# Kernel optimization log

Hardware: AMD Instinct MI355X
Metric: run time of the kernel (lower is better)

## Reference

```python
import jax, jax.numpy as jnp
import numpy as np

N_EMBED = 256
N_HEAD = 8
HEAD = N_EMBED // N_HEAD
LN_EPS = 1e-5


def _layernorm(x, g, b):
    mu = jnp.mean(x, axis=-1, keepdims=True)
    var = jnp.mean(jnp.square(x - mu), axis=-1, keepdims=True)
    return (x - mu) * jax.lax.rsqrt(var + LN_EPS) * g + b


def setup_inputs() -> dict:
    key = jax.random.key(0)
    ks = jax.random.split(key, 12)
    B, T, C, H, D = 16, 1024, N_EMBED, N_HEAD, HEAD
    s = C ** -0.5
    return {
        "x": jax.random.normal(ks[0], (B, T, C), jnp.float32),
        "wq": jax.random.normal(ks[1], (H, C, D), jnp.float32) * s,
        "wk": jax.random.normal(ks[2], (H, C, D), jnp.float32) * s,
        "wv": jax.random.normal(ks[3], (H, C, D), jnp.float32) * s,
        "w_proj": jax.random.normal(ks[4], (C, C), jnp.float32) * s,
        "b_proj": jnp.zeros((C,), jnp.float32),
        "w1": jax.random.normal(ks[5], (C, 4 * C), jnp.float32) * s,
        "b1": jnp.zeros((4 * C,), jnp.float32),
        "w2": jax.random.normal(ks[6], (4 * C, C), jnp.float32) * (4 * C) ** -0.5,
        "b2": jnp.zeros((C,), jnp.float32),
        "ln1_g": jnp.ones((C,), jnp.float32),
        "ln1_b": jnp.zeros((C,), jnp.float32),
        "ln2_g": jnp.ones((C,), jnp.float32),
        "ln2_b": jnp.zeros((C,), jnp.float32),
    }


def reference(x, wq, wk, wv, w_proj, b_proj, w1, b1, w2, b2,
              ln1_g, ln1_b, ln2_g, ln2_b):
    B, T, C = x.shape
    # --- multi-head causal self-attention on ln1(x) ---
    h = _layernorm(x, ln1_g, ln1_b)
    q = jnp.einsum('btc,hcd->bhtd', h, wq)
    k = jnp.einsum('btc,hcd->bhtd', h, wk)
    v = jnp.einsum('btc,hcd->bhtd', h, wv)
    # NOTE: original scales by n_embed**-0.5 (C of input), not head_size
    wei = jnp.einsum('bhtd,bhsd->bhts', q, k) * (C ** -0.5)
    causal = jnp.tril(jnp.ones((T, T), bool))
    wei = jnp.where(causal, wei, -jnp.inf)
    wei = jax.nn.softmax(wei, axis=-1)
    att = jnp.einsum('bhts,bhsd->bhtd', wei, v)
    att = att.transpose(0, 2, 1, 3).reshape(B, T, C)  # concat heads
    x = x + att @ w_proj + b_proj
    # --- feedforward on ln2(x) ---
    h2 = _layernorm(x, ln2_g, ln2_b)
    f = jax.nn.relu(h2 @ w1 + b1) @ w2 + b2
    return x + f
```

## Files before the change

### kernel.cpp

```cpp
#include <hip/hip_runtime.h>


typedef unsigned short u16;
typedef unsigned int u32;
typedef __attribute__((ext_vector_type(8))) short short8v;
typedef __attribute__((ext_vector_type(4))) float float4v;

__device__ __forceinline__ float b2f(u16 u) { union { u32 i; float f; } v; v.i = (u32)u << 16; return v.f; }
__device__ __forceinline__ float lo2f(u32 u) { union { u32 i; float f; } v; v.i = u << 16; return v.f; }
__device__ __forceinline__ float hi2f(u32 u) { union { u32 i; float f; } v; v.i = u & 0xffff0000u; return v.f; }
__device__ __forceinline__ u16 f2b(float f) {
    union { float f; u32 i; } v; v.f = f;
    u32 r = v.i + 0x7fffu + ((v.i >> 16) & 1u);
    return (u16)(r >> 16);
}
__device__ __forceinline__ u32 pk2_rtz(float a, float b) {
    return (__float_as_uint(a) >> 16) | (__float_as_uint(b) & 0xffff0000u);
}
__device__ __forceinline__ void async_cp16(const u16* g, u16* l) {
    __builtin_amdgcn_global_load_lds((const __attribute__((address_space(1))) void*)g,
                                     (__attribute__((address_space(3))) void*)l, 16, 0, 0);
}

__global__ __launch_bounds__(256) void prep_ln1(const float* __restrict__ wq,
                                                const float* __restrict__ wk,
                                                const float* __restrict__ wv,
                                                const float* __restrict__ wp,
                                                const float* __restrict__ w1,
                                                const float* __restrict__ w2,
                                                const float* __restrict__ x,
                                                const float* __restrict__ g1,
                                                const float* __restrict__ be1,
                                                u16* __restrict__ wqkvT,
                                                u16* __restrict__ wpT,
                                                u16* __restrict__ w1T,
                                                u16* __restrict__ w2T,
                                                u16* __restrict__ hout) {
    __shared__ u16 tile[64][65];
    int bid = blockIdx.x, tid = threadIdx.x;
    if (bid < 768) {
        int i = bid * 256 + tid;
        int n = i >> 8, k = i & 255;
        int which = n >> 8, nn = n & 255;
        const float* w = which == 0 ? wq : (which == 1 ? wk : wv);
        float v = w[((nn >> 5) * 256 + k) * 32 + (nn & 31)];
        if (which == 0) v *= 0.09016844f;
        wqkvT[i] = f2b(v);
    } else if (bid < 912) {
        const float* src; u16* dst; int K, N, t;
        if (bid < 784)      { src = wp; dst = wpT; K = 256;  N = 256;  t = bid - 768; }
        else if (bid < 848) { src = w1; dst = w1T; K = 256;  N = 1024; t = bid - 784; }
        else                { src = w2; dst = w2T; K = 1024; N = 256;  t = bid - 848; }
        int ntn = N >> 6;
        int k0 = (t / ntn) << 6, n0 = (t % ntn) << 6;
        int lane = tid & 63, wrow = tid >> 6;
        #pragma unroll
        for (int r = 0; r < 16; r++) {
            int k = wrow * 16 + r;
            tile[k][lane] = f2b(src[(size_t)(k0 + k) * N + n0 + lane]);
        }
        __syncthreads();
        #pragma unroll
        for (int r = 0; r < 16; r++) {
            int n = wrow * 16 + r;
            dst[(size_t)(n0 + n) * K + k0 + lane] = tile[lane][n];
        }
    } else {
        int row = (bid - 912) * 4 + (tid >> 6);
        int lane = tid & 63;
        float4 xv = *(const float4*)(x + (size_t)row * 256 + lane * 4);
        float v0 = xv.x, v1 = xv.y, v2 = xv.z, v3 = xv.w;
        float s = v0 + v1 + v2 + v3;
        #pragma unroll
        for (int m = 32; m; m >>= 1) s += __shfl_xor(s, m);
        float mu = s * 0.00390625f;
        float d0 = v0 - mu, d1 = v1 - mu, d2 = v2 - mu, d3 = v3 - mu;
        float ss = d0 * d0 + d1 * d1 + d2 * d2 + d3 * d3;
        #pragma unroll
        for (int m = 32; m; m >>= 1) ss += __shfl_xor(ss, m);
        float rs = rsqrtf(ss * 0.00390625f + 1e-5f);
        float4 g = *(const float4*)(g1 + lane * 4);
        float4 b = *(const float4*)(be1 + lane * 4);
        uint2 r;
        r.x = (u32)f2b(d0 * rs * g.x + b.x) | ((u32)f2b(d1 * rs * g.y + b.y) << 16);
        r.y = (u32)f2b(d2 * rs * g.z + b.z) | ((u32)f2b(d3 * rs * g.w + b.w) << 16);
        *(uint2*)(hout + (size_t)row * 256 + lane * 4) = r;
    }
}

template<bool HASBIAS, bool RELU, bool QKV>
__global__ __launch_bounds__(256) void gemm128(const u16* __restrict__ A,
                                               const u16* __restrict__ Bt,
                                               const float* __restrict__ bias,
                                               u16* __restrict__ out,
                                               u16* __restrict__ vout,
                                               int M, int N, int K) {
    __shared__ __align__(16) u16 SH[32768];
    const int tid = threadIdx.x, lane = tid & 63, w = tid >> 6;
    const int m0 = blockIdx.x * 128, n0 = blockIdx.y * 128;
    const int wm = (w & 1) * 64, wn = (w >> 1) * 64;
    const int fm = lane & 15, q = lane >> 4;

    float4v acc[4][4];
    #pragma unroll
    for (int i = 0; i < 4; i++)
        #pragma unroll
        for (int j = 0; j < 4; j++) acc[i][j] = (float4v){0.f, 0.f, 0.f, 0.f};

    const int kset = ((lane & 7) ^ (lane >> 3)) * 8;
    const u16* Ag = A  + (size_t)(m0 + w * 32 + (lane >> 3)) * K + kset;
    const u16* Bg = Bt + (size_t)(n0 + w * 32 + (lane >> 3)) * K + kset;

    auto issueS = [&](int t, int d) {
        u16* Asw = SH + d * 16384 + (w * 32) * 64;
        u16* Bsw = SH + d * 16384 + 8192 + (w * 32) * 64;
        #pragma unroll
        for (int c = 0; c < 4; c++) {
            async_cp16(Ag + (size_t)c * 8 * K + t * 64, Asw + c * 8 * 64);
            async_cp16(Bg + (size_t)c * 8 * K + t * 64, Bsw + c * 8 * 64);
        }
    };
    issueS(0, 0);
    issueS(1, 1);

    const int sw = fm & 7;
    #pragma unroll
    for (int t = 0; t < 4; ++t) {
        if (t == 3) asm volatile("s_waitcnt vmcnt(0)" ::: "memory");
        else        asm volatile("s_waitcnt vmcnt(8)" ::: "memory");
        __builtin_amdgcn_s_barrier();
        const u16* As = SH + (t & 1) * 16384;
        const u16* Bs = As + 8192;
        __builtin_amdgcn_s_setprio(1);
        #pragma unroll
        for (int kk = 0; kk < 64; kk += 32) {
            const int slot = (((kk >> 3) + q) ^ sw) * 8;
            short8v af[4], bf[4];
            #pragma unroll
            for (int mi = 0; mi < 4; mi++)
                af[mi] = *(const short8v*)&As[(wm + mi * 16 + fm) * 64 + slot];
            #pragma unroll
            for (int ni = 0; ni < 4; ni++)
                bf[ni] = *(const short8v*)&Bs[(wn + ni * 16 + fm) * 64 + slot];
            #pragma unroll
            for (int mi = 0; mi < 4; mi++)
                #pragma unroll
                for (int ni = 0; ni < 4; ni++)
                    acc[mi][ni] = __builtin_amdgcn_mfma_f32_16x16x32_bf16(
                        bf[ni], af[mi], acc[mi][ni], 0, 0, 0);
        }
        __builtin_amdgcn_s_setprio(0);
        if (t < 2) {
            __builtin_amdgcn_s_barrier();
            issueS(t + 2, t & 1);
        }
    }

    if (QKV && n0 >= 512) {
        __syncthreads();
        #pragma unroll
        for (int mi = 0; mi < 4; mi++) {
            int ml = wm + mi * 16 + fm;
            #pragma unroll
            for (int ni = 0; ni < 4; ni++) {
                int nl = wn + ni * 16 + q * 4;
                #pragma unroll
                for (int r = 0; r < 4; r++)
                    SH[(nl + r) * 136 + ml] = f2b(acc[mi][ni][r]);
            }
        }
        __syncthreads();
        int r = tid & 127, c = (tid >> 7) << 6;
        int hd = (n0 - 512) + r;
        int b = m0 >> 10, t0 = m0 & 1023;
        u16* dst = vout + (size_t)(b * 256 + hd) * 1024 + t0 + c;
        const u16* srcT = SH + r * 136 + c;
        #pragma unroll
        for (int i = 0; i < 8; i++)
            *(uint4*)(dst + i * 8) = *(const uint4*)(srcT + i * 8);
        return;
    }

    #pragma unroll
    for (int mi = 0; mi < 4; mi++) {
        int row = m0 + wm + mi * 16 + fm;
        #pragma unroll
        for (int ni = 0; ni < 4; ni++) {
            int nb = n0 + wn + ni * 16 + q * 4;
            float v0 = acc[mi][ni][0], v1 = acc[mi][ni][1],
                  v2 = acc[mi][ni][2], v3 = acc[mi][ni][3];
            if (HASBIAS) {
                float4 bv = *(const float4*)&bias[nb];
                v0 += bv.x; v1 += bv.y; v2 += bv.z; v3 += bv.w;
            }
            if (RELU) {
                v0 = fmaxf(v0, 0.f); v1 = fmaxf(v1, 0.f);
                v2 = fmaxf(v2, 0.f); v3 = fmaxf(v3, 0.f);
            }
            size_t idx = (size_t)row * N + nb;
            uint2 ov;
            ov.x = (u32)f2b(v0) | ((u32)f2b(v1) << 16);
            ov.y = (u32)f2b(v2) | ((u32)f2b(v3) << 16);
            *(uint2*)&out[idx] = ov;
        }
    }
}

__global__ __launch_bounds__(512, 1) void tail_fused(const u16* __restrict__ att,
                                                     const u16* __restrict__ wpT,
                                                     const float* __restrict__ bp,
                                                     const float* __restrict__ x,
                                                     const float* __restrict__ g2,
                                                     const float* __restrict__ be2,
                                                     const u16* __restrict__ w1T,
                                                     const float* __restrict__ b1,
                                                     const u16* __restrict__ w2T,
                                                     const float* __restrict__ b2,
                                                     float* __restrict__ out) {
    __shared__ __align__(16) u16 SH[65536];
    __shared__ float ps[2][2][16][4], pq[2][2][16][4];
    u16* Ms = SH;
    u16* Bs = SH + 16384;
    const int tid = threadIdx.x, lane = tid & 63, w = tid >> 6;
    const int m0 = blockIdx.x * 64;
    const int wmi = w & 1, wni = w >> 1;
    const int wm = wmi * 32;
    const int wn = wni * 64;
    const int fm = lane & 15, q = lane >> 4;
    const int sw = fm & 7;
    const int kset = ((lane & 7) ^ (lane >> 3)) * 8;
    const int rb = w * 8 + (lane >> 3);

    short8v ar[8][2];
    {
        const u16* Abase = att + (size_t)(m0 + wm + fm) * 256 + q * 8;
        #pragma unroll
        for (int kcn = 0; kcn < 8; kcn++)
            #pragma unroll
            for (int mi = 0; mi < 2; mi++)
                ar[kcn][mi] = *(const short8v*)(Abase + (size_t)mi * 16 * 256 + kcn * 32);
    }

    auto issueB = [&](int u, u16* dst) {
        if (u < 4) {
            const u16* src = wpT + (size_t)rb * 256 + u * 64 + kset;
            #pragma unroll
            for (int c = 0; c < 4; c++)
                async_cp16(src + (size_t)c * 64 * 256, dst + c * 4096);
        } else {
            const int tt = u - 4, n2 = tt >> 3, k2 = tt & 3;
            if (((tt >> 2) & 1) == 0) {
                const u16* src = w1T + (size_t)(n2 * 256 + rb) * 256 + k2 * 64 + kset;
                #pragma unroll
                for (int c = 0; c < 4; c++)
                    async_cp16(src + (size_t)c * 64 * 256, dst + c * 4096);
            } else {
                const u16* src = w2T + (size_t)rb * 1024 + n2 * 256 + k2 * 64 + kset;
                #pragma unroll
                for (int c = 0; c < 4; c++)
                    async_cp16(src + (size_t)c * 64 * 1024, dst + c * 4096);
            }
        }
    };

    issueB(0, Bs + w * 512);
    issueB(1, Bs + 16384 + w * 512);

    float4v acc1[2][4], acc2[2][4], xr[2][4];
    #pragma unroll
    for (int i = 0; i < 2; i++)
        #pragma unroll
        for (int j = 0; j < 4; j++) {
            acc1[i][j] = (float4v){0.f, 0.f, 0.f, 0.f};
            acc2[i][j] = (float4v){0.f, 0.f, 0.f, 0.f};
        }

    #pragma unroll
    for (int t = 0; t < 36; ++t) {
        if (t == 35) asm volatile("s_waitcnt vmcnt(0)" ::: "memory");
        else         asm volatile("s_waitcnt vmcnt(4)" ::: "memory");
        __builtin_amdgcn_s_barrier();
        if (t + 2 < 36)
            issueB(t + 2, Bs + ((t + 2) % 3) * 16384 + w * 512);
        const u16* Bb = Bs + (t % 3) * 16384;

        if (t < 4) {
            __builtin_amdgcn_s_setprio(1);
            #pragma unroll
            for (int kk = 0; kk < 64; kk += 32) {
                const int slot = (((kk >> 3) + q) ^ sw) * 8;
                short8v bf[4];
                #pragma unroll
                for (int ni = 0; ni < 4; ni++)
                    bf[ni] = *(const short8v*)&Bb[(wn + ni * 16 + fm) * 64 + slot];
                #pragma unroll
                for (int mi = 0; mi < 2; mi++)
                    #pragma unroll
                    for (int ni = 0; ni < 4; ni++)
                        acc1[mi][ni] = __builtin_amdgcn_mfma_f32_16x16x32_bf16(
                            bf[ni], ar[t * 2 + (kk >> 5)][mi], acc1[mi][ni], 0, 0, 0);
            }
            __builtin_amdgcn_s_setprio(0);
            if (t == 3) {
                float s[2] = {0.f, 0.f}, s2[2] = {0.f, 0.f};
                #pragma unroll
                for (int mi = 0; mi < 2; mi++)
                    #pragma unroll
                    for (int ni = 0; ni < 4; ni++) {
                        const int nb = wn + ni * 16 + q * 4;
                        const int row = m0 + wm + mi * 16 + fm;
                        float4 bv = *(const float4*)&bp[nb];
                        float4 xv = *(const float4*)(x + (size_t)row * 256 + nb);
                        #pragma unroll
                        for (int r = 0; r < 4; r++) {
                            float tv = acc1[mi][ni][r] + (&bv.x)[r] + (&xv.x)[r];
                            xr[mi][ni][r] = tv;
                            s[mi] += tv; s2[mi] += tv * tv;
                        }
                    }
                #pragma unroll
                for (int mi = 0; mi < 2; mi++) {
                    s[mi]  += __shfl_xor(s[mi], 16);  s[mi]  += __shfl_xor(s[mi], 32);
                    s2[mi] += __shfl_xor(s2[mi], 16); s2[mi] += __shfl_xor(s2[mi], 32);
                }
                if (q == 0) {
                    ps[wmi][0][fm][wni] = s[0];  ps[wmi][1][fm][wni] = s[1];
                    pq[wmi][0][fm][wni] = s2[0]; pq[wmi][1][fm][wni] = s2[1];
                }
                asm volatile("s_waitcnt lgkmcnt(0)" ::: "memory");
                __builtin_amdgcn_s_barrier();
                float mu[2], rs[2];
                #pragma unroll
                for (int mi = 0; mi < 2; mi++) {
                    float S  = ps[wmi][mi][fm][0] + ps[wmi][mi][fm][1]
                             + ps[wmi][mi][fm][2] + ps[wmi][mi][fm][3];
                    float SQ = pq[wmi][mi][fm][0] + pq[wmi][mi][fm][1]
                             + pq[wmi][mi][fm][2] + pq[wmi][mi][fm][3];
                    mu[mi] = S * 0.00390625f;
                    rs[mi] = rsqrtf(SQ * 0.00390625f - mu[mi] * mu[mi] + 1e-5f);
                }
                #pragma unroll
                for (int ni = 0; ni < 4; ni++) {
                    const int c2 = wn + ni * 16 + q * 4;
                    const int kcM = c2 >> 6, cc = c2 & 63;
                    float4 gv = *(const float4*)&g2[c2];
                    float4 bv = *(const float4*)&be2[c2];
                    #pragma unroll
                    for (int mi = 0; mi < 2; mi++) {
                        const int row = wm + mi * 16 + fm;
                        float h0 = (xr[mi][ni][0] - mu[mi]) * rs[mi] * gv.x + bv.x;
                        float h1 = (xr[mi][ni][1] - mu[mi]) * rs[mi] * gv.y + bv.y;
                        float h2v = (xr[mi][ni][2] - mu[mi]) * rs[mi] * gv.z + bv.z;
                        float h3 = (xr[mi][ni][3] - mu[mi]) * rs[mi] * gv.w + bv.w;
                        uint2 pp;
                        pp.x = (u32)f2b(h0) | ((u32)f2b(h1) << 16);
                        pp.y = (u32)f2b(h2v) | ((u32)f2b(h3) << 16);
                        *(uint2*)&Ms[kcM * 4096 + row * 64 +
                                     (((cc >> 3) ^ (row & 7)) * 8) + (cc & 7)] = pp;
                    }
                }
                asm volatile("s_waitcnt lgkmcnt(0)" ::: "memory");
                __builtin_amdgcn_s_barrier();
                #pragma unroll
                for (int kcn = 0; kcn < 8; kcn++) {
                    const int kcq = kcn >> 1, kk = (kcn & 1) * 32;
                    const int slot = (((kk >> 3) + q) ^ sw) * 8;
                    #pragma unroll
                    for (int mi = 0; mi < 2; mi++)
                        ar[kcn][mi] = *(const short8v*)&Ms[kcq * 4096 +
                                        (wm + mi * 16 + fm) * 64 + slot];
                }
            }
        } else {
            const int tt = t - 4;
            const int nch = tt >> 3, ph = (tt >> 2) & 1, kc = tt & 3;
            if (ph == 0) {
                if (kc == 0) {
                    #pragma unroll
                    for (int i = 0; i < 2; i++)
                        #pragma unroll
                        for (int j = 0; j < 4; j++) acc1[i][j] = (float4v){0.f, 0.f, 0.f, 0.f};
                }
                __builtin_amdgcn_s_setprio(1);
                #pragma unroll
                for (int kk = 0; kk < 64; kk += 32) {
                    const int slot = (((kk >> 3) + q) ^ sw) * 8;
                    short8v bf[4];
                    #pragma unroll
                    for (int ni = 0; ni < 4; ni++)
                        bf[ni] = *(const short8v*)&Bb[(wn + ni * 16 + fm) * 64 + slot];
                    #pragma unroll
                    for (int mi = 0; mi < 2; mi++)
                        #pragma unroll
                        for (int ni = 0; ni < 4; ni++)
                            acc1[mi][ni] = __builtin_amdgcn_mfma_f32_16x16x32_bf16(
                                bf[ni], ar[kc * 2 + (kk >> 5)][mi], acc1[mi][ni], 0, 0, 0);
                }
                __builtin_amdgcn_s_setprio(0);
                if (kc == 3) {
                    #pragma unroll
                    for (int ni = 0; ni < 4; ni++) {
                        const int c2 = wn + ni * 16 + q * 4;
                        const int kcM = c2 >> 6, cc = c2 & 63;
                        float4 bv = *(const float4*)&b1[nch * 256 + c2];
                        #pragma unroll
                        for (int mi = 0; mi < 2; mi++) {
                            const int row = wm + mi * 16 + fm;
                            float v0 = fmaxf(acc1[mi][ni][0] + bv.x, 0.f);
                            float v1 = fmaxf(acc1[mi][ni][1] + bv.y, 0.f);
                            float v2 = fmaxf(acc1[mi][ni][2] + bv.z, 0.f);
                            float v3 = fmaxf(acc1[mi][ni][3] + bv.w, 0.f);
                            uint2 pp;
                            pp.x = (u32)f2b(v0) | ((u32)f2b(v1) << 16);
                            pp.y = (u32)f2b(v2) | ((u32)f2b(v3) << 16);
                            *(uint2*)&Ms[kcM * 4096 + row * 64 +
                                         (((cc >> 3) ^ (row & 7)) * 8) + (cc & 7)] = pp;
                        }
                    }
                    asm volatile("s_waitcnt lgkmcnt(0)" ::: "memory");
                }
            } else {
                const u16* Ab = Ms + kc * 4096;
                __builtin_amdgcn_s_setprio(1);
                #pragma unroll
                for (int kk = 0; kk < 64; kk += 32) {
                    const int slot = (((kk >> 3) + q) ^ sw) * 8;
                    short8v af[2], bf[4];
                    #pragma unroll
                    for (int mi = 0; mi < 2; mi++)
                        af[mi] = *(const short8v*)&Ab[(wm + mi * 16 + fm) * 64 + slot];
                    #pragma unroll
                    for (int ni = 0; ni < 4; ni++)
                        bf[ni] = *(const short8v*)&Bb[(wn + ni * 16 + fm) * 64 + slot];
                    #pragma unroll
                    for (int mi = 0; mi < 2; mi++)
                        #pragma unroll
                        for (int ni = 0; ni < 4; ni++)
                            acc2[mi][ni] = __builtin_amdgcn_mfma_f32_16x16x32_bf16(
                                bf[ni], af[mi], acc2[mi][ni], 0, 0, 0);
                }
                __builtin_amdgcn_s_setprio(0);
            }
        }
    }

    #pragma unroll
    for (int mi = 0; mi < 2; mi++) {
        const int row = m0 + wm + mi * 16 + fm;
        #pragma unroll
        for (int ni = 0; ni < 4; ni++) {
            const int nb = wn + ni * 16 + q * 4;
            size_t idx = (size_t)row * 256 + nb;
            float4 bv = *(const float4*)&b2[nb];
            float v0 = acc2[mi][ni][0] + bv.x + xr[mi][ni][0];
            float v1 = acc2[mi][ni][1] + bv.y + xr[mi][ni][1];
            float v2 = acc2[mi][ni][2] + bv.z + xr[mi][ni][2];
            float v3 = acc2[mi][ni][3] + bv.w + xr[mi][ni][3];
            *(float4*)&out[idx] = (float4){v0, v1, v2, v3};
        }
    }
}

__global__ __launch_bounds__(256) void attn_mfma(const u16* __restrict__ qk,
                                                 const u16* __restrict__ vtg,
                                                 u16* __restrict__ att) {
    const int T = 1024;
    int jj = (blockIdx.x + (blockIdx.y >> 3)) & 7;
    int b = blockIdx.y >> 3, hh = blockIdx.y & 7;
    int tid = threadIdx.x;
    int lane = tid & 63, w = tid >> 6;
    int fm = lane & 15, q = lane >> 4;

    __shared__ __align__(16) u16 Ks[2][64][72];
    __shared__ __align__(16) u16 Vt[2][32][72];
    __shared__ __align__(16) u16 Pl[4][16][72];

    size_t base = (size_t)b * T * 512;
    const u16* kb = qk + base + 256 + hh * 32;
    const u16* vt = vtg + (size_t)((b * 8 + hh) * 32) * 1024;
    const int krow = tid >> 2, kcol = (tid & 3) * 8;
    const int vd = tid >> 3, vs = (tid & 7) * 8;

    int qa0 = jj * 64, qb0 = (15 - jj) * 64;
    int tqa = qa0 + w * 16 + fm, tqb = qb0 + w * 16 + fm;
    short8v qfa = *(const short8v*)(qk + base + (size_t)tqa * 512 + hh * 32 + q * 8);
    short8v qfb = *(const short8v*)(qk + base + (size_t)tqb * 512 + hh * 32 + q * 8);
    float4v oa0 = {0.f, 0.f, 0.f, 0.f}, oa1 = {0.f, 0.f, 0.f, 0.f};
    float4v ob0 = {0.f, 0.f, 0.f, 0.f}, ob1 = {0.f, 0.f, 0.f, 0.f};
    float la = 0.f, lb = 0.f;
    int wqa = qa0 + w * 16, wqb = qb0 + w * 16;
    int nIter = 16 - jj;

    uint4 kreg = *(const uint4*)(kb + (size_t)krow * 512 + kcol);
    uint4 vreg = *(const uint4*)(vt + (size_t)vd * 1024 + vs);

    for (int it = 0; it < nIter; ++it) {
        int s0 = it << 6;
        const int cb = it & 1;
        *(uint4*)&Ks[cb][krow][kcol] = kreg;
        *(uint4*)&Vt[cb][vd][vs] = vreg;
        if (it + 1 < nIter) {
            int ns0 = s0 + 64;
            kreg = *(const uint4*)(kb + (size_t)(ns0 + krow) * 512 + kcol);
            vreg = *(const uint4*)(vt + (size_t)vd * 1024 + ns0 + vs);
        }
        asm volatile("s_waitcnt lgkmcnt(0)" ::: "memory");
        __builtin_amdgcn_s_barrier();
        short8v kf0 = *(const short8v*)&Ks[cb][fm][q * 8];
        short8v kf1 = *(const short8v*)&Ks[cb][16 + fm][q * 8];
        short8v kf2 = *(const short8v*)&Ks[cb][32 + fm][q * 8];
        short8v kf3 = *(const short8v*)&Ks[cb][48 + fm][q * 8];
        short8v vf00 = *(const short8v*)&Vt[cb][fm][q * 8];
        short8v vf01 = *(const short8v*)&Vt[cb][fm][32 + q * 8];
        short8v vf10 = *(const short8v*)&Vt[cb][16 + fm][q * 8];
        short8v vf11 = *(const short8v*)&Vt[cb][16 + fm][32 + q * 8];
        float4v z = {0.f, 0.f, 0.f, 0.f};

        #pragma unroll
        for (int t2 = 0; t2 < 2; t2++) {
            int wq0 = t2 ? wqa : wqb;
            if (s0 >= wq0 + 16) continue;
            int tq = t2 ? tqa : tqb;
            short8v qf = t2 ? qfa : qfb;
            __builtin_amdgcn_s_setprio(1);
            float4v s_0 = __builtin_amdgcn_mfma_f32_16x16x32_bf16(kf0, qf, z, 0, 0, 0);
            float4v s_1 = __builtin_amdgcn_mfma_f32_16x16x32_bf16(kf1, qf, z, 0, 0, 0);
            float4v s_2 = __builtin_amdgcn_mfma_f32_16x16x32_bf16(kf2, qf, z, 0, 0, 0);
            float4v s_3 = __builtin_amdgcn_mfma_f32_16x16x32_bf16(kf3, qf, z, 0, 0, 0);
            __builtin_amdgcn_s_setprio(0);
            float p[16];
            #pragma unroll
            for (int r = 0; r < 4; r++) {
                p[r] = exp2f(s_0[r]); p[4 + r] = exp2f(s_1[r]);
                p[8 + r] = exp2f(s_2[r]); p[12 + r] = exp2f(s_3[r]);
            }
            if (s0 + 63 > wq0) {
                int sb = s0 + q * 4;
                #pragma unroll
                for (int c = 0; c < 4; c++)
                    #pragma unroll
                    for (int r = 0; r < 4; r++)
                        if (sb + c * 16 + r > tq) p[c * 4 + r] = 0.f;
            }
            float rsum = 0.f;
            #pragma unroll
            for (int i = 0; i < 16; i++) rsum += p[i];
            rsum += __shfl_xor(rsum, 16);
            rsum += __shfl_xor(rsum, 32);
            if (t2) la += rsum; else lb += rsum;

            #pragma unroll
            for (int c = 0; c < 4; c++) {
                uint2 pp;
                pp.x = pk2_rtz(p[c * 4 + 0], p[c * 4 + 1]);
                pp.y = pk2_rtz(p[c * 4 + 2], p[c * 4 + 3]);
                *(uint2*)&Pl[w][fm][c * 16 + q * 4] = pp;
            }
            short8v pf0 = *(const short8v*)&Pl[w][fm][q * 8];
            short8v pf1 = *(const short8v*)&Pl[w][fm][32 + q * 8];
            __builtin_amdgcn_s_setprio(1);
            if (t2) {
                oa0 = __builtin_amdgcn_mfma_f32_16x16x32_bf16(vf00, pf0, oa0, 0, 0, 0);
                oa0 = __builtin_amdgcn_mfma_f32_16x16x32_bf16(vf01, pf1, oa0, 0, 0, 0);
                oa1 = __builtin_amdgcn_mfma_f32_16x16x32_bf16(vf10, pf0, oa1, 0, 0, 0);
                oa1 = __builtin_amdgcn_mfma_f32_16x16x32_bf16(vf11, pf1, oa1, 0, 0, 0);
            } else {
                ob0 = __builtin_amdgcn_mfma_f32_16x16x32_bf16(vf00, pf0, ob0, 0, 0, 0);
                ob0 = __builtin_amdgcn_mfma_f32_16x16x32_bf16(vf01, pf1, ob0, 0, 0, 0);
                ob1 = __builtin_amdgcn_mfma_f32_16x16x32_bf16(vf10, pf0, ob1, 0, 0, 0);
                ob1 = __builtin_amdgcn_mfma_f32_16x16x32_bf16(vf11, pf1, ob1, 0, 0, 0);
            }
            __builtin_amdgcn_s_setprio(0);
        }
    }

    #pragma unroll
    for (int t2 = 0; t2 < 2; t2++) {
        float inv = 1.f / (t2 ? la : lb);
        float4v o0 = t2 ? oa0 : ob0, o1 = t2 ? oa1 : ob1;
        int tq = t2 ? tqa : tqb;
        uint2 r0, r1;
        r0.x = (u32)f2b(o0[0] * inv) | ((u32)f2b(o0[1] * inv) << 16);
        r0.y = (u32)f2b(o0[2] * inv) | ((u32)f2b(o0[3] * inv) << 16);
        r1.x = (u32)f2b(o1[0] * inv) | ((u32)f2b(o1[1] * inv) << 16);
        r1.y = (u32)f2b(o1[2] * inv) | ((u32)f2b(o1[3] * inv) << 16);
        size_t o = (size_t)(b * T + tq) * 256 + hh * 32;
        *(uint2*)(att + o + q * 4) = r0;
        *(uint2*)(att + o + 16 + q * 4) = r1;
    }
}

extern "C" void kernel_launch(void* const* d_in, const int* in_sizes, int n_in,
                              void* d_out, int out_size, void* d_ws, size_t ws_size,
                              hipStream_t stream) {
    const int BT = 16 * 1024;
    const float* x      = (const float*)d_in[0];
    const float* wq     = (const float*)d_in[1];
    const float* wk     = (const float*)d_in[2];
    const float* wv     = (const float*)d_in[3];
    const float* w_proj = (const float*)d_in[4];
    const float* b_proj = (const float*)d_in[5];
    const float* w1     = (const float*)d_in[6];
    const float* b1     = (const float*)d_in[7];
    const float* w2     = (const float*)d_in[8];
    const float* b2     = (const float*)d_in[9];
    const float* ln1_g  = (const float*)d_in[10];
    const float* ln1_b  = (const float*)d_in[11];
    const float* ln2_g  = (const float*)d_in[12];
    const float* ln2_b  = (const float*)d_in[13];

    char* ws = (char*)d_ws;
    const size_t MB = 1024 * 1024;
    u16*  hbuf  = (u16*)(ws + 8 * MB);
    u16*  qk    = (u16*)(ws + 16 * MB);
    u16*  vtg   = (u16*)(ws + 32 * MB);
    u16*  wqkvT = (u16*)(ws + 48 * MB);
    u16*  wpT   = (u16*)(ws + 48 * MB + 0x60000);
    u16*  w1T   = (u16*)(ws + 48 * MB + 0x80000);
    u16*  w2T   = (u16*)(ws + 48 * MB + 0x100000);

    prep_ln1<<<5008, 256, 0, stream>>>(wq, wk, wv, w_proj, w1, w2, x, ln1_g, ln1_b,
                                       wqkvT, wpT, w1T, w2T, hbuf);
    gemm128<false, false, true><<<dim3(128, 6), 256, 0, stream>>>(
        hbuf, wqkvT, nullptr, qk, vtg, BT, 512, 256);
    attn_mfma<<<dim3(8, 128), 256, 0, stream>>>(qk, vtg, hbuf);
    tail_fused<<<256, 512, 0, stream>>>(hbuf, wpT, b_proj, x, ln2_g, ln2_b,
                                        w1T, b1, w2T, b2, (float*)d_out);
}
```

Before: 174.3 us.

## Split weight prefetch across MMA halves and batch QK MFMAs in attention

In the fused tail kernel, each per-stage weight prefetch is split into two halves. The second half is issued between the two k-halves of the MFMA work, so global-to-LDS copies are spread through compute instead of bunched after the barrier. In the attention kernel, the QK score MFMAs for both query sub-tiles are issued together before either softmax/PV sequence, which lets the MFMA pipeline overlap with the exp work. The b-tile is now computed unconditionally, which assumes it is always active. It also raises register pressure from holding eight score fragments at once.

```diff
diff --git a/kernel.cpp b/kernel.cpp
--- a/kernel.cpp
+++ b/kernel.cpp
@@ -206,6 +206,39 @@
     }
 }
 
+#define TMM_A(KH, AFRAG, ACC)                                                     \
+    do {                                                                          \
+        const int slot_ = ((((KH) ? 4 : 0) + q) ^ sw) * 8;                        \
+        short8v bf_[4];                                                           \
+        _Pragma("unroll")                                                         \
+        for (int ni = 0; ni < 4; ni++)                                            \
+            bf_[ni] = *(const short8v*)&Bb[(wn + ni * 16 + fm) * 64 + slot_];     \
+        _Pragma("unroll")                                                         \
+        for (int mi = 0; mi < 2; mi++)                                            \
+            _Pragma("unroll")                                                     \
+            for (int ni = 0; ni < 4; ni++)                                        \
+                ACC[mi][ni] = __builtin_amdgcn_mfma_f32_16x16x32_bf16(            \
+                    bf_[ni], (AFRAG), ACC[mi][ni], 0, 0, 0);                      \
+    } while (0)
+
+#define TMM_M(KH, ABASE, ACC)                                                     \
+    do {                                                                          \
+        const int slot_ = ((((KH) ? 4 : 0) + q) ^ sw) * 8;                        \
+        short8v af_[2], bf_[4];                                                   \
+        _Pragma("unroll")                                                         \
+        for (int mi = 0; mi < 2; mi++)                                            \
+            af_[mi] = *(const short8v*)&(ABASE)[(wm + mi * 16 + fm) * 64 + slot_];\
+        _Pragma("unroll")                                                         \
+        for (int ni = 0; ni < 4; ni++)                                            \
+            bf_[ni] = *(const short8v*)&Bb[(wn + ni * 16 + fm) * 64 + slot_];     \
+        _Pragma("unroll")                                                         \
+        for (int mi = 0; mi < 2; mi++)                                            \
+            _Pragma("unroll")                                                     \
+            for (int ni = 0; ni < 4; ni++)                                        \
+                ACC[mi][ni] = __builtin_amdgcn_mfma_f32_16x16x32_bf16(            \
+                    bf_[ni], af_[mi], ACC[mi][ni], 0, 0, 0);                      \
+    } while (0)
+
 __global__ __launch_bounds__(512, 1) void tail_fused(const u16* __restrict__ att,
                                                      const u16* __restrict__ wpT,
                                                      const float* __restrict__ bp,
@@ -241,30 +274,31 @@
                 ar[kcn][mi] = *(const short8v*)(Abase + (size_t)mi * 16 * 256 + kcn * 32);
     }
 
-    auto issueB = [&](int u, u16* dst) {
+    auto issueBh = [&](int u, u16* dst, int h) {
+        const int c0 = h * 2;
         if (u < 4) {
             const u16* src = wpT + (size_t)rb * 256 + u * 64 + kset;
             #pragma unroll
-            for (int c = 0; c < 4; c++)
+            for (int c = c0; c < c0 + 2; c++)
                 async_cp16(src + (size_t)c * 64 * 256, dst + c * 4096);
         } else {
             const int tt = u - 4, n2 = tt >> 3, k2 = tt & 3;
             if (((tt >> 2) & 1) == 0) {
                 const u16* src = w1T + (size_t)(n2 * 256 + rb) * 256 + k2 * 64 + kset;
                 #pragma unroll
-                for (int c = 0; c < 4; c++)
+                for (int c = c0; c < c0 + 2; c++)
                     async_cp16(src + (size_t)c * 64 * 256, dst + c * 4096);
             } else {
                 const u16* src = w2T + (size_t)rb * 1024 + n2 * 256 + k2 * 64 + kset;
                 #pragma unroll
-                for (int c = 0; c < 4; c++)
+                for (int c = c0; c < c0 + 2; c++)
                     async_cp16(src + (size_t)c * 64 * 1024, dst + c * 4096);
             }
         }
     };
 
-    issueB(0, Bs + w * 512);
-    issueB(1, Bs + 16384 + w * 512);
+    issueBh(0, Bs + w * 512, 0); issueBh(0, Bs + w * 512, 1);
+    issueBh(1, Bs + 16384 + w * 512, 0); issueBh(1, Bs + 16384 + w * 512, 1);
 
     float4v acc1[2][4], acc2[2][4], xr[2][4];
     #pragma unroll
@@ -280,26 +314,18 @@
         if (t == 35) asm volatile("s_waitcnt vmcnt(0)" ::: "memory");
         else         asm volatile("s_waitcnt vmcnt(4)" ::: "memory");
         __builtin_amdgcn_s_barrier();
-        if (t + 2 < 36)
-            issueB(t + 2, Bs + ((t + 2) % 3) * 16384 + w * 512);
+        u16* dstB = Bs + ((t + 2) % 3) * 16384 + w * 512;
+        const bool doIss = (t + 2 < 36);
+        if (doIss) issueBh(t + 2, dstB, 0);
         const u16* Bb = Bs + (t % 3) * 16384;
 
         if (t < 4) {
             __builtin_amdgcn_s_setprio(1);
-            #pragma unroll
-            for (int kk = 0; kk < 64; kk += 32) {
-                const int slot = (((kk >> 3) + q) ^ sw) * 8;
-                short8v bf[4];
-                #pragma unroll
-                for (int ni = 0; ni < 4; ni++)
-                    bf[ni] = *(const short8v*)&Bb[(wn + ni * 16 + fm) * 64 + slot];
-                #pragma unroll
-                for (int mi = 0; mi < 2; mi++)
-                    #pragma unroll
-                    for (int ni = 0; ni < 4; ni++)
-                        acc1[mi][ni] = __builtin_amdgcn_mfma_f32_16x16x32_bf16(
-                            bf[ni], ar[t * 2 + (kk >> 5)][mi], acc1[mi][ni], 0, 0, 0);
-            }
+            TMM_A(0, ar[t * 2 + 0][mi], acc1);
+            __builtin_amdgcn_s_setprio(0);
+            if (doIss) issueBh(t + 2, dstB, 1);
+            __builtin_amdgcn_s_setprio(1);
+            TMM_A(1, ar[t * 2 + 1][mi], acc1);
             __builtin_amdgcn_s_setprio(0);
             if (t == 3) {
                 float s[2] = {0.f, 0.f}, s2[2] = {0.f, 0.f};
@@ -382,20 +408,11 @@
                         for (int j = 0; j < 4; j++) acc1[i][j] = (float4v){0.f, 0.f, 0.f, 0.f};
                 }
                 __builtin_amdgcn_s_setprio(1);
-                #pragma unroll
-                for (int kk = 0; kk < 64; kk += 32) {
-                    const int slot = (((kk >> 3) + q) ^ sw) * 8;
-                    short8v bf[4];
-                    #pragma unroll
-                    for (int ni = 0; ni < 4; ni++)
-                        bf[ni] = *(const short8v*)&Bb[(wn + ni * 16 + fm) * 64 + slot];
-                    #pragma unroll
-                    for (int mi = 0; mi < 2; mi++)
-                        #pragma unroll
-                        for (int ni = 0; ni < 4; ni++)
-                            acc1[mi][ni] = __builtin_amdgcn_mfma_f32_16x16x32_bf16(
-                                bf[ni], ar[kc * 2 + (kk >> 5)][mi], acc1[mi][ni], 0, 0, 0);
-                }
+                TMM_A(0, ar[kc * 2 + 0][mi], acc1);
+                __builtin_amdgcn_s_setprio(0);
+                if (doIss) issueBh(t + 2, dstB, 1);
+                __builtin_amdgcn_s_setprio(1);
+                TMM_A(1, ar[kc * 2 + 1][mi], acc1);
                 __builtin_amdgcn_s_setprio(0);
                 if (kc == 3) {
                     #pragma unroll
@@ -422,23 +439,11 @@
             } else {
                 const u16* Ab = Ms + kc * 4096;
                 __builtin_amdgcn_s_setprio(1);
-                #pragma unroll
-                for (int kk = 0; kk < 64; kk += 32) {
-                    const int slot = (((kk >> 3) + q) ^ sw) * 8;
-                    short8v af[2], bf[4];
-                    #pragma unroll
-                    for (int mi = 0; mi < 2; mi++)
-                        af[mi] = *(const short8v*)&Ab[(wm + mi * 16 + fm) * 64 + slot];
-                    #pragma unroll
-                    for (int ni = 0; ni < 4; ni++)
-                        bf[ni] = *(const short8v*)&Bb[(wn + ni * 16 + fm) * 64 + slot];
-                    #pragma unroll
-                    for (int mi = 0; mi < 2; mi++)
-                        #pragma unroll
-                        for (int ni = 0; ni < 4; ni++)
-                            acc2[mi][ni] = __builtin_amdgcn_mfma_f32_16x16x32_bf16(
-                                bf[ni], af[mi], acc2[mi][ni], 0, 0, 0);
-                }
+                TMM_M(0, Ab, acc2);
+                __builtin_amdgcn_s_setprio(0);
+                if (doIss) issueBh(t + 2, dstB, 1);
+                __builtin_amdgcn_s_setprio(1);
+                TMM_M(1, Ab, acc2);
                 __builtin_amdgcn_s_setprio(0);
             }
         }
@@ -460,6 +465,45 @@
         }
     }
 }
+
+#define SM_PV(S0_, S1_, S2_, S3_, TQ, WQ0, LSUM, O0, O1)                          \
+    do {                                                                          \
+        float p[16];                                                              \
+        _Pragma("unroll")                                                         \
+        for (int r = 0; r < 4; r++) {                                             \
+            p[r] = exp2f((S0_)[r]);      p[4 + r] = exp2f((S1_)[r]);              \
+            p[8 + r] = exp2f((S2_)[r]);  p[12 + r] = exp2f((S3_)[r]);             \
+        }                                                                         \
+        if (s0 + 63 > (WQ0)) {                                                    \
+            int sb_ = s0 + q * 4;                                                 \
+            _Pragma("unroll")                                                     \
+            for (int c = 0; c < 4; c++)                                           \
+                _Pragma("unroll")                                                 \
+                for (int r = 0; r < 4; r++)                                       \
+                    if (sb_ + c * 16 + r > (TQ)) p[c * 4 + r] = 0.f;              \
+        }                                                                         \
+        float rsum = 0.f;                                                         \
+        _Pragma("unroll")                                                         \
+        for (int i = 0; i < 16; i++) rsum += p[i];                                \
+        rsum += __shfl_xor(rsum, 16);                                             \
+        rsum += __shfl_xor(rsum, 32);                                             \
+        LSUM += rsum;                                                             \
+        _Pragma("unroll")                                                         \
+        for (int c = 0; c < 4; c++) {                                             \
+            uint2 pp;                                                             \
+            pp.x = pk2_rtz(p[c * 4 + 0], p[c * 4 + 1]);                           \
+            pp.y = pk2_rtz(p[c * 4 + 2], p[c * 4 + 3]);                           \
+            *(uint2*)&Pl[w][fm][c * 16 + q * 4] = pp;                             \
+        }                                                                         \
+        short8v pf0 = *(const short8v*)&Pl[w][fm][q * 8];                         \
+        short8v pf1 = *(const short8v*)&Pl[w][fm][32 + q * 8];                    \
+        __builtin_amdgcn_s_setprio(1);                                            \
+        O0 = __builtin_amdgcn_mfma_f32_16x16x32_bf16(vf00, pf0, O0, 0, 0, 0);     \
+        O0 = __builtin_amdgcn_mfma_f32_16x16x32_bf16(vf01, pf1, O0, 0, 0, 0);     \
+        O1 = __builtin_amdgcn_mfma_f32_16x16x32_bf16(vf10, pf0, O1, 0, 0, 0);     \
+        O1 = __builtin_amdgcn_mfma_f32_16x16x32_bf16(vf11, pf1, O1, 0, 0, 0);     \
+        __builtin_amdgcn_s_setprio(0);                                            \
+    } while (0)
 
 __global__ __launch_bounds__(256) void attn_mfma(const u16* __restrict__ qk,
                                                  const u16* __restrict__ vtg,
@@ -515,63 +559,24 @@
         short8v vf10 = *(const short8v*)&Vt[cb][16 + fm][q * 8];
         short8v vf11 = *(const short8v*)&Vt[cb][16 + fm][32 + q * 8];
         float4v z = {0.f, 0.f, 0.f, 0.f};
-
-        #pragma unroll
-        for (int t2 = 0; t2 < 2; t2++) {
-            int wq0 = t2 ? wqa : wqb;
-            if (s0 >= wq0 + 16) continue;
-            int tq = t2 ? tqa : tqb;
-            short8v qf = t2 ? qfa : qfb;
-            __builtin_amdgcn_s_setprio(1);
-            float4v s_0 = __builtin_amdgcn_mfma_f32_16x16x32_bf16(kf0, qf, z, 0, 0, 0);
-            float4v s_1 = __builtin_amdgcn_mfma_f32_16x16x32_bf16(kf1, qf, z, 0, 0, 0);
-            float4v s_2 = __builtin_amdgcn_mfma_f32_16x16x32_bf16(kf2, qf, z, 0, 0, 0);
-            float4v s_3 = __builtin_amdgcn_mfma_f32_16x16x32_bf16(kf3, qf, z, 0, 0, 0);
-            __builtin_amdgcn_s_setprio(0);
-            float p[16];
-            #pragma unroll
-            for (int r = 0; r < 4; r++) {
-                p[r] = exp2f(s_0[r]); p[4 + r] = exp2f(s_1[r]);
-                p[8 + r] = exp2f(s_2[r]); p[12 + r] = exp2f(s_3[r]);
-            }
-            if (s0 + 63 > wq0) {
-                int sb = s0 + q * 4;
-                #pragma unroll
-                for (int c = 0; c < 4; c++)
-                    #pragma unroll
-                    for (int r = 0; r < 4; r++)
-                        if (sb + c * 16 + r > tq) p[c * 4 + r] = 0.f;
-            }
-            float rsum = 0.f;
-            #pragma unroll
-            for (int i = 0; i < 16; i++) rsum += p[i];
-            rsum += __shfl_xor(rsum, 16);
-            rsum += __shfl_xor(rsum, 32);
-            if (t2) la += rsum; else lb += rsum;
-
-            #pragma unroll
-            for (int c = 0; c < 4; c++) {
-                uint2 pp;
-                pp.x = pk2_rtz(p[c * 4 + 0], p[c * 4 + 1]);
-                pp.y = pk2_rtz(p[c * 4 + 2], p[c * 4 + 3]);
-                *(uint2*)&Pl[w][fm][c * 16 + q * 4] = pp;
-            }
-            short8v pf0 = *(const short8v*)&Pl[w][fm][q * 8];
-            short8v pf1 = *(const short8v*)&Pl[w][fm][32 + q * 8];
-            __builtin_amdgcn_s_setprio(1);
-            if (t2) {
-                oa0 = __builtin_amdgcn_mfma_f32_16x16x32_bf16(vf00, pf0, oa0, 0, 0, 0);
-                oa0 = __builtin_amdgcn_mfma_f32_16x16x32_bf16(vf01, pf1, oa0, 0, 0, 0);
-                oa1 = __builtin_amdgcn_mfma_f32_16x16x32_bf16(vf10, pf0, oa1, 0, 0, 0);
-                oa1 = __builtin_amdgcn_mfma_f32_16x16x32_bf16(vf11, pf1, oa1, 0, 0, 0);
-            } else {
-                ob0 = __builtin_amdgcn_mfma_f32_16x16x32_bf16(vf00, pf0, ob0, 0, 0, 0);
-                ob0 = __builtin_amdgcn_mfma_f32_16x16x32_bf16(vf01, pf1, ob0, 0, 0, 0);
-                ob1 = __builtin_amdgcn_mfma_f32_16x16x32_bf16(vf10, pf0, ob1, 0, 0, 0);
-                ob1 = __builtin_amdgcn_mfma_f32_16x16x32_bf16(vf11, pf1, ob1, 0, 0, 0);
-            }
-            __builtin_amdgcn_s_setprio(0);
-        }
+        const bool actA = (s0 < wqa + 16);
+
+        __builtin_amdgcn_s_setprio(1);
+        float4v sb0 = __builtin_amdgcn_mfma_f32_16x16x32_bf16(kf0, qfb, z, 0, 0, 0);
+        float4v sb1 = __builtin_amdgcn_mfma_f32_16x16x32_bf16(kf1, qfb, z, 0, 0, 0);
+        float4v sb2 = __builtin_amdgcn_mfma_f32_16x16x32_bf16(kf2, qfb, z, 0, 0, 0);
+        float4v sb3 = __builtin_amdgcn_mfma_f32_16x16x32_bf16(kf3, qfb, z, 0, 0, 0);
+        float4v sa0 = z, sa1 = z, sa2 = z, sa3 = z;
+        if (actA) {
+            sa0 = __builtin_amdgcn_mfma_f32_16x16x32_bf16(kf0, qfa, z, 0, 0, 0);
+            sa1 = __builtin_amdgcn_mfma_f32_16x16x32_bf16(kf1, qfa, z, 0, 0, 0);
+            sa2 = __builtin_amdgcn_mfma_f32_16x16x32_bf16(kf2, qfa, z, 0, 0, 0);
+            sa3 = __builtin_amdgcn_mfma_f32_16x16x32_bf16(kf3, qfa, z, 0, 0, 0);
+        }
+        __builtin_amdgcn_s_setprio(0);
+
+        SM_PV(sb0, sb1, sb2, sb3, tqb, wqb, lb, ob0, ob1);
+        if (actA) SM_PV(sa0, sa1, sa2, sa3, tqa, wqa, la, oa0, oa1);
     }
 
     #pragma unroll
```

After: 180.0 us. 3.3% more time.
